# Performance work log

Measured on AMD Instinct MI355X. Metric: run time of the kernel, lower is better.

Reference implementation:

```python
import jax, jax.numpy as jnp
import numpy as np

K = 128
T_X = 4
DATA_LENGTH = 512
B_GROUPS = 64
B = B_GROUPS * DATA_LENGTH
INV_SQRT2 = 0.7071067811865476  # 1/sqrt(2), haar reconstruction filter coeff


def setup_inputs() -> dict:
    key = jax.random.key(0)
    ks = jax.random.split(key, 9)
    x = jax.random.normal(ks[0], (B, T_X, K), jnp.float32)
    y = jax.random.normal(ks[1], (B, 1, K), jnp.float32)
    s = 1.0 / np.sqrt(K).astype(np.float32)
    Wq = jax.random.normal(ks[2], (K, K), jnp.float32) * s
    Wk = jax.random.normal(ks[3], (K, K), jnp.float32) * s
    Wv = jax.random.normal(ks[4], (K, K), jnp.float32) * s
    conv_w = jax.random.normal(ks[5], (K, 2 * K), jnp.float32) * (1.0 / np.sqrt(2 * K).astype(np.float32))
    conv_b = jax.random.normal(ks[6], (K,), jnp.float32) * 0.01
    bn_gamma = jnp.ones((K,), jnp.float32)
    bn_beta = jnp.zeros((K,), jnp.float32)
    bn_mean = jax.random.normal(ks[7], (K,), jnp.float32) * 0.1
    bn_var = jax.random.uniform(ks[8], (K,), jnp.float32, 0.5, 1.5)
    return dict(x=x, y=y, Wq=Wq, Wk=Wk, Wv=Wv, conv_w=conv_w, conv_b=conv_b,
                bn_gamma=bn_gamma, bn_beta=bn_beta, bn_mean=bn_mean, bn_var=bn_var,
                data_length=DATA_LENGTH)


def _idwt_haar(L, H):
    # inverse 1D haar transform along last dim: (Bg, C, 1, T) -> (Bg, C, 1, 2T)
    even = (L + H) * INV_SQRT2
    odd = (L - H) * INV_SQRT2
    out = jnp.stack([even, odd], axis=-1)  # (..., T, 2)
    return out.reshape(L.shape[:-1] + (L.shape[-1] * 2,))


def reference(x, y, Wq, Wk, Wv, conv_w, conv_b, bn_gamma, bn_beta, bn_mean, bn_var, data_length):
    b, t_x, k = x.shape  # t_x = 4 bands, heads = 1, t_y = 1
    q = jnp.einsum('btk,ok->bto', y, Wq)                      # (b, 1, k)
    keys = jnp.einsum('bsk,ok->bso', x, Wk) * (1.0 / (k ** 0.5))  # (b, 4, k)
    v = jnp.einsum('bsk,ok->bso', x, Wv)                      # (b, 4, k)
    dot = jnp.einsum('bto,bso->bs', q, keys)                  # (b, 4)
    w = jax.nn.softmax(dot, axis=1)                           # softmax over the 4 bands
    outs = w[:, :, None] * v                                  # (b, 4, k) band-weighted values
    Bg = b // data_length
    # per band: (b, k) -> (Bg, dl, 1, k) -> permute -> (Bg, k, 1, dl)
    o = outs.reshape(Bg, data_length, t_x, k).transpose(2, 0, 3, 1)  # (4, Bg, k, dl)
    o = o[:, :, :, None, :]                                   # (4, Bg, k, 1, dl)
    out_L = _idwt_haar(o[0], o[1])                            # (Bg, k, 1, 2*dl)
    out_H = _idwt_haar(o[2], o[3])
    out = jnp.concatenate([out_L, out_H], axis=1)             # (Bg, 2k, 1, 2*dl)
    # transition: 1x1 conv + BN (eval mode) + LeakyReLU(0.01)
    z = jnp.einsum('bcij,oc->boij', out, conv_w) + conv_b[None, :, None, None]
    scale = (bn_gamma * jax.lax.rsqrt(bn_var + 1e-5))[None, :, None, None]
    z = (z - bn_mean[None, :, None, None]) * scale + bn_beta[None, :, None, None]
    return jnp.where(z > 0, z, 0.01 * z)
```

## Files before the change

kernel.cpp:

```cpp
#include <hip/hip_runtime.h>
#include <stdint.h>

typedef __attribute__((ext_vector_type(8))) short bf16x8;
typedef __attribute__((ext_vector_type(4))) float f32x4;

__device__ __forceinline__ unsigned short f2bf(float x) {
    union { float f; uint32_t u; } v; v.f = x;
    uint32_t r = v.u + 0x7FFFu + ((v.u >> 16) & 1u);
    return (unsigned short)(r >> 16);
}
__device__ __forceinline__ uint32_t pack2bf(float a, float b) {
    return (uint32_t)f2bf(a) | ((uint32_t)f2bf(b) << 16);
}
__device__ __forceinline__ uint32_t cvtpk(float a, float b) {
    uint32_t r;
    asm("v_cvt_pk_bf16_f32 %0, %1, %2" : "=v"(r) : "v"(a), "v"(b));
    return r;
}
__device__ __forceinline__ float bf2f(uint32_t lo) {
    union { uint32_t u; float f; } v; v.u = lo << 16; return v.f;
}
__device__ __forceinline__ float lrelu(float v) { return v > 0.f ? v : 0.01f * v; }

__global__ __launch_bounds__(256) void precompute_kernel(
    const float* __restrict__ Wq, const float* __restrict__ Wk,
    const float* __restrict__ Wv, const float* __restrict__ conv_w,
    const float* __restrict__ conv_b, const float* __restrict__ bn_gamma,
    const float* __restrict__ bn_beta, const float* __restrict__ bn_mean,
    const float* __restrict__ bn_var,
    unsigned short* __restrict__ Gh, unsigned short* __restrict__ Gl,
    unsigned short* __restrict__ Mh,
    float* __restrict__ scale2, float* __restrict__ bias2)
{
    __shared__ float lds0[2176];
    __shared__ float lds1[2176];
    const int tid = threadIdx.x;
    const int bid = blockIdx.x;

    if (bid == 192) {
        if (tid < 128) {
            float sc = bn_gamma[tid] * rsqrtf(bn_var[tid] + 1e-5f);
            scale2[tid] = sc;
            bias2[tid]  = (conv_b[tid] - bn_mean[tid]) * sc + bn_beta[tid];
        }
        return;
    }

    if (bid < 64) {
        int i0 = (bid >> 3) << 4, j0 = (bid & 7) << 4;
        #pragma unroll
        for (int t = 0; t < 8; ++t) {
            int e = tid + t * 256;
            int o = e >> 4, c = e & 15;
            lds0[o * 17 + c] = Wk[o * 128 + i0 + c];
            lds1[o * 17 + c] = Wq[o * 128 + j0 + c];
        }
        __syncthreads();
        int ti = tid >> 4, tj = tid & 15;
        float sum = 0.f;
        #pragma unroll 8
        for (int o = 0; o < 128; ++o) sum += lds0[o * 17 + ti] * lds1[o * 17 + tj];
        float val = sum * 0.08838834764831845f;
        unsigned short h = f2bf(val);
        int idx = (i0 + ti) * 128 + j0 + tj;
        Gh[idx] = h;
        Gl[idx] = f2bf(val - bf2f(h));
    } else {
        int rel = bid - 64;
        int o0 = (rel >> 4) << 4, c0 = (rel & 15) << 4;
        int cw0 = (c0 >> 7) << 7, cc0 = c0 & 127;
        #pragma unroll
        for (int t = 0; t < 8; ++t) {
            int e = tid + t * 256;
            int to = e >> 7, k = e & 127;
            lds0[to * 132 + k] = conv_w[(o0 + to) * 256 + cw0 + k];
            int kk = e >> 4, c = e & 15;
            lds1[kk * 17 + c] = Wv[kk * 128 + cc0 + c];
        }
        __syncthreads();
        int to = tid >> 4, tc = tid & 15;
        float sum = 0.f;
        #pragma unroll 8
        for (int k = 0; k < 128; ++k) sum += lds0[to * 132 + k] * lds1[k * 17 + tc];
        Mh[(o0 + to) * 256 + c0 + tc] = f2bf(sum * 0.7071067811865476f);
    }
}

#define AADDR(row, gi)   (((row) << 8) + ((((gi) ^ ((row) & 7))) << 4))

__global__ __launch_bounds__(256)
__attribute__((amdgpu_waves_per_eu(3)))
void fused_kernel(
    const float* __restrict__ x, const float* __restrict__ y,
    const unsigned short* __restrict__ Gh, const unsigned short* __restrict__ Gl,
    const unsigned short* __restrict__ Mh,
    const float* __restrict__ scale2, const float* __restrict__ bias2,
    float* __restrict__ out)
{
    __shared__ __align__(16) unsigned char smem[32768];
    float* gbufF = (float*)(smem + 16384);

    const int tid = threadIdx.x;
    const int w = tid >> 6;
    const int l = tid & 63;
    const int quad = l >> 4;
    const int i16 = l & 15;
    const int bid = blockIdx.x;
    const int b0 = bid * 32;

    float4 yv0[2], yv1[2];
    int rowA[2], gkA[2];
    #pragma unroll
    for (int it = 0; it < 2; ++it) {
        int j = tid + it * 256;
        rowA[it] = j >> 4; gkA[it] = j & 15;
        const float* yb = y + (size_t)(b0 + rowA[it]) * 128 + gkA[it] * 8;
        yv0[it] = *(const float4*)(yb);
        yv1[it] = *(const float4*)(yb + 4);
    }
    bf16x8 pgh[4][2], pgl[4][2];
    #pragma unroll
    for (int ks = 0; ks < 4; ++ks) {
        int ksr = (ks + bid) & 3;
        #pragma unroll
        for (int n = 0; n < 2; ++n) {
            int off = ((2 * w + n) * 16 + i16) * 128 + ksr * 32 + quad * 8;
            pgh[ks][n] = *(const bf16x8*)(Gh + off);
            pgl[ks][n] = *(const bf16x8*)(Gl + off);
        }
    }
    union F8 { float4 v[2]; float f[8]; };
    F8 X[2][4];
    #pragma unroll
    for (int pass = 0; pass < 2; ++pass) {
        int b_loc = 8 * w + pass * 4 + quad;
        const float* xb = x + (size_t)(b0 + b_loc) * 512 + i16 * 8;
        #pragma unroll
        for (int t = 0; t < 4; ++t) {
            X[pass][t].v[0] = *(const float4*)(xb + t * 128);
            X[pass][t].v[1] = *(const float4*)(xb + t * 128 + 4);
        }
    }

    #pragma unroll
    for (int it = 0; it < 2; ++it) {
        float f[8] = {yv0[it].x, yv0[it].y, yv0[it].z, yv0[it].w,
                      yv1[it].x, yv1[it].y, yv1[it].z, yv1[it].w};
        uint32_t hi[4], lo[4];
        #pragma unroll
        for (int e = 0; e < 4; ++e) {
            unsigned short h0 = f2bf(f[2 * e]), h1 = f2bf(f[2 * e + 1]);
            hi[e] = (uint32_t)h0 | ((uint32_t)h1 << 16);
            lo[e] = (uint32_t)f2bf(f[2 * e] - bf2f(h0)) |
                    ((uint32_t)f2bf(f[2 * e + 1] - bf2f(h1)) << 16);
        }
        int addr = AADDR(rowA[it], gkA[it]);
        *(uint4*)(smem + addr)        = make_uint4(hi[0], hi[1], hi[2], hi[3]);
        *(uint4*)(smem + 8192 + addr) = make_uint4(lo[0], lo[1], lo[2], lo[3]);
    }
    __syncthreads();

    {
        f32x4 accg[2][2];
        #pragma unroll
        for (int rt = 0; rt < 2; ++rt)
            #pragma unroll
            for (int n = 0; n < 2; ++n) accg[rt][n] = (f32x4){0.f, 0.f, 0.f, 0.f};
        #pragma unroll
        for (int ks = 0; ks < 4; ++ks) {
            int ksr = (ks + bid) & 3;
            bf16x8 ah[2], al[2];
            #pragma unroll
            for (int rt = 0; rt < 2; ++rt) {
                int row = 16 * rt + i16;
                int addr = AADDR(row, ksr * 4 + quad);
                ah[rt] = *(const bf16x8*)(smem + addr);
                al[rt] = *(const bf16x8*)(smem + 8192 + addr);
            }
            #pragma unroll
            for (int n = 0; n < 2; ++n) {
                #pragma unroll
                for (int rt = 0; rt < 2; ++rt) {
                    accg[rt][n] = __builtin_amdgcn_mfma_f32_16x16x32_bf16(ah[rt], pgh[ks][n], accg[rt][n], 0, 0, 0);
                    accg[rt][n] = __builtin_amdgcn_mfma_f32_16x16x32_bf16(al[rt], pgh[ks][n], accg[rt][n], 0, 0, 0);
                    accg[rt][n] = __builtin_amdgcn_mfma_f32_16x16x32_bf16(ah[rt], pgl[ks][n], accg[rt][n], 0, 0, 0);
                }
            }
        }
        #pragma unroll
        for (int n = 0; n < 2; ++n) {
            int i = (2 * w + n) * 16 + i16;
            #pragma unroll
            for (int rt = 0; rt < 2; ++rt)
                #pragma unroll
                for (int r = 0; r < 4; ++r)
                    gbufF[(16 * rt + quad * 4 + r) * 128 + i] = accg[rt][n][r];
        }
    }
    __syncthreads();

    #pragma unroll
    for (int pass = 0; pass < 2; ++pass) {
        int b_loc = 8 * w + pass * 4 + quad;
        float4 ga = *(const float4*)(gbufF + b_loc * 128 + i16 * 8);
        float4 gb = *(const float4*)(gbufF + b_loc * 128 + i16 * 8 + 4);
        float p[4];
        #pragma unroll
        for (int t = 0; t < 4; ++t) {
            float4 a = X[pass][t].v[0], b = X[pass][t].v[1];
            p[t] = a.x * ga.x + a.y * ga.y + a.z * ga.z + a.w * ga.w
                 + b.x * gb.x + b.y * gb.y + b.z * gb.z + b.w * gb.w;
        }
        #pragma unroll
        for (int off = 8; off >= 1; off >>= 1) {
            p[0] += __shfl_xor(p[0], off);
            p[1] += __shfl_xor(p[1], off);
            p[2] += __shfl_xor(p[2], off);
            p[3] += __shfl_xor(p[3], off);
        }
        float mx = fmaxf(fmaxf(p[0], p[1]), fmaxf(p[2], p[3]));
        float e0 = __expf(p[0] - mx), e1 = __expf(p[1] - mx);
        float e2 = __expf(p[2] - mx), e3 = __expf(p[3] - mx);
        float inv = 1.f / (e0 + e1 + e2 + e3);
        float w0 = e0 * inv, w1 = e1 * inv, w2 = e2 * inv, w3 = e3 * inv;
        int r0 = 2 * b_loc, r1 = r0 + 1;
        int a0 = AADDR(r0, i16), a1 = AADDR(r1, i16);
        uint32_t eL[4], oL[4], eH[4], oH[4];
        #pragma unroll
        for (int e = 0; e < 4; ++e) {
            int c0 = 2 * e, c1 = 2 * e + 1;
            eL[e] = cvtpk(w0 * X[pass][0].f[c0] + w1 * X[pass][1].f[c0], w0 * X[pass][0].f[c1] + w1 * X[pass][1].f[c1]);
            oL[e] = cvtpk(w0 * X[pass][0].f[c0] - w1 * X[pass][1].f[c0], w0 * X[pass][0].f[c1] - w1 * X[pass][1].f[c1]);
            eH[e] = cvtpk(w2 * X[pass][2].f[c0] + w3 * X[pass][3].f[c0], w2 * X[pass][2].f[c1] + w3 * X[pass][3].f[c1]);
            oH[e] = cvtpk(w2 * X[pass][2].f[c0] - w3 * X[pass][3].f[c0], w2 * X[pass][2].f[c1] - w3 * X[pass][3].f[c1]);
        }
        *(uint4*)(smem + a0)         = make_uint4(eL[0], eL[1], eL[2], eL[3]);
        *(uint4*)(smem + a1)         = make_uint4(oL[0], oL[1], oL[2], oL[3]);
        *(uint4*)(smem + 16384 + a0) = make_uint4(eH[0], eH[1], eH[2], eH[3]);
        *(uint4*)(smem + 16384 + a1) = make_uint4(oH[0], oH[1], oH[2], oH[3]);
    }

    const int ks0b = bid & 7;
    bf16x8 pmh[2];
    {
        int half = ks0b >> 2, kk = ks0b & 3;
        #pragma unroll
        for (int n = 0; n < 2; ++n)
            pmh[n] = *(const bf16x8*)(Mh + ((2 * w + n) * 16 + i16) * 256 + half * 128 + kk * 32 + quad * 8);
    }
    __syncthreads();

    f32x4 acc[4][2];
    #pragma unroll
    for (int rb = 0; rb < 4; ++rb)
        #pragma unroll
        for (int n = 0; n < 2; ++n) acc[rb][n] = (f32x4){0.f, 0.f, 0.f, 0.f};

    #pragma unroll
    for (int ks = 0; ks < 8; ++ks) {
        int ksr = (ks + bid) & 7;
        int half = ksr >> 2, kk = ksr & 3;
        int base = half << 14;
        int gi = kk * 4 + quad;
        bf16x8 a[4];
        #pragma unroll
        for (int rb = 0; rb < 4; ++rb)
            a[rb] = *(const bf16x8*)(smem + base + AADDR(16 * rb + i16, gi));
        #pragma unroll
        for (int n = 0; n < 2; ++n) {
            bf16x8 bh;
            if (ks == 0) bh = pmh[n];
            else bh = *(const bf16x8*)(Mh + ((2 * w + n) * 16 + i16) * 256 + half * 128 + kk * 32 + quad * 8);
            #pragma unroll
            for (int rb = 0; rb < 4; ++rb)
                acc[rb][n] = __builtin_amdgcn_mfma_f32_16x16x32_bf16(a[rb], bh, acc[rb][n], 0, 0, 0);
        }
    }

    {
        float* outp = out + (size_t)(bid >> 4) * 131072 + (bid & 15) * 64;
        #pragma unroll
        for (int n = 0; n < 2; ++n) {
            int o = (2 * w + n) * 16 + i16;
            float sc = scale2[o], bi = bias2[o];
            #pragma unroll
            for (int rb = 0; rb < 4; ++rb) {
                int jb = 16 * rb + quad * 4;
                f32x4 a = acc[rb][n];
                float4 r;
                r.x = lrelu(a[0] * sc + bi);
                r.y = lrelu(a[1] * sc + bi);
                r.z = lrelu(a[2] * sc + bi);
                r.w = lrelu(a[3] * sc + bi);
                *(float4*)(outp + (size_t)o * 1024 + jb) = r;
            }
        }
    }
}

extern "C" void kernel_launch(void* const* d_in, const int* in_sizes, int n_in,
                              void* d_out, int out_size, void* d_ws, size_t ws_size,
                              hipStream_t stream)
{
    (void)in_sizes; (void)n_in; (void)out_size; (void)ws_size;
    const float* x        = (const float*)d_in[0];
    const float* y        = (const float*)d_in[1];
    const float* Wq       = (const float*)d_in[2];
    const float* Wk       = (const float*)d_in[3];
    const float* Wv       = (const float*)d_in[4];
    const float* conv_w   = (const float*)d_in[5];
    const float* conv_b   = (const float*)d_in[6];
    const float* bn_gamma = (const float*)d_in[7];
    const float* bn_beta  = (const float*)d_in[8];
    const float* bn_mean  = (const float*)d_in[9];
    const float* bn_var   = (const float*)d_in[10];

    unsigned char* ws = (unsigned char*)d_ws;
    unsigned short* Gh = (unsigned short*)(ws);
    unsigned short* Gl = (unsigned short*)(ws + 32768);
    unsigned short* Mh = (unsigned short*)(ws + 65536);
    float* scale2      = (float*)(ws + 131072);
    float* bias2       = (float*)(ws + 131584);

    hipLaunchKernelGGL(precompute_kernel, dim3(193), dim3(256), 0, stream,
                       Wq, Wk, Wv, conv_w, conv_b, bn_gamma, bn_beta, bn_mean,
                       bn_var, Gh, Gl, Mh, scale2, bias2);
    hipLaunchKernelGGL(fused_kernel, dim3(1024), dim3(256), 0, stream,
                       x, y, Gh, Gl, Mh, scale2, bias2, (float*)d_out);
}
```

Measured before the change: 149.5 us.

## Split fused kernel into softmax-weight kernel and IDWT/conv kernel

Result: slower. 156.7 us (+4.8%).

```diff
diff --git a/kernel.cpp b/kernel.cpp
--- a/kernel.cpp
+++ b/kernel.cpp
@@ -8,9 +8,6 @@
     union { float f; uint32_t u; } v; v.f = x;
     uint32_t r = v.u + 0x7FFFu + ((v.u >> 16) & 1u);
     return (unsigned short)(r >> 16);
-}
-__device__ __forceinline__ uint32_t pack2bf(float a, float b) {
-    return (uint32_t)f2bf(a) | ((uint32_t)f2bf(b) << 16);
 }
 __device__ __forceinline__ uint32_t cvtpk(float a, float b) {
     uint32_t r;
@@ -89,13 +86,11 @@
 #define AADDR(row, gi)   (((row) << 8) + ((((gi) ^ ((row) & 7))) << 4))
 
 __global__ __launch_bounds__(256)
-__attribute__((amdgpu_waves_per_eu(3)))
-void fused_kernel(
+__attribute__((amdgpu_waves_per_eu(4)))
+void dot_kernel(
     const float* __restrict__ x, const float* __restrict__ y,
     const unsigned short* __restrict__ Gh, const unsigned short* __restrict__ Gl,
-    const unsigned short* __restrict__ Mh,
-    const float* __restrict__ scale2, const float* __restrict__ bias2,
-    float* __restrict__ out)
+    float* __restrict__ wbuf)
 {
     __shared__ __align__(16) unsigned char smem[32768];
     float* gbufF = (float*)(smem + 16384);
@@ -127,18 +122,6 @@
             int off = ((2 * w + n) * 16 + i16) * 128 + ksr * 32 + quad * 8;
             pgh[ks][n] = *(const bf16x8*)(Gh + off);
             pgl[ks][n] = *(const bf16x8*)(Gl + off);
-        }
-    }
-    union F8 { float4 v[2]; float f[8]; };
-    F8 X[2][4];
-    #pragma unroll
-    for (int pass = 0; pass < 2; ++pass) {
-        int b_loc = 8 * w + pass * 4 + quad;
-        const float* xb = x + (size_t)(b0 + b_loc) * 512 + i16 * 8;
-        #pragma unroll
-        for (int t = 0; t < 4; ++t) {
-            X[pass][t].v[0] = *(const float4*)(xb + t * 128);
-            X[pass][t].v[1] = *(const float4*)(xb + t * 128 + 4);
         }
     }
 
@@ -204,10 +187,12 @@
         int b_loc = 8 * w + pass * 4 + quad;
         float4 ga = *(const float4*)(gbufF + b_loc * 128 + i16 * 8);
         float4 gb = *(const float4*)(gbufF + b_loc * 128 + i16 * 8 + 4);
+        const float* xb = x + (size_t)(b0 + b_loc) * 512 + i16 * 8;
         float p[4];
         #pragma unroll
         for (int t = 0; t < 4; ++t) {
-            float4 a = X[pass][t].v[0], b = X[pass][t].v[1];
+            float4 a = *(const float4*)(xb + t * 128);
+            float4 b = *(const float4*)(xb + t * 128 + 4);
             p[t] = a.x * ga.x + a.y * ga.y + a.z * ga.z + a.w * ga.w
                  + b.x * gb.x + b.y * gb.y + b.z * gb.z + b.w * gb.w;
         }
@@ -222,17 +207,52 @@
         float e0 = __expf(p[0] - mx), e1 = __expf(p[1] - mx);
         float e2 = __expf(p[2] - mx), e3 = __expf(p[3] - mx);
         float inv = 1.f / (e0 + e1 + e2 + e3);
-        float w0 = e0 * inv, w1 = e1 * inv, w2 = e2 * inv, w3 = e3 * inv;
+        if (i16 == 0) {
+            float4 wv = make_float4(e0 * inv, e1 * inv, e2 * inv, e3 * inv);
+            *(float4*)(wbuf + (size_t)(b0 + b_loc) * 4) = wv;
+        }
+    }
+}
+
+__global__ __launch_bounds__(256) void u_kernel(
+    const float* __restrict__ x, const float* __restrict__ wbuf,
+    const unsigned short* __restrict__ Mh,
+    const float* __restrict__ scale2, const float* __restrict__ bias2,
+    float* __restrict__ out)
+{
+    __shared__ __align__(16) unsigned char smem[32768];
+    const int tid = threadIdx.x;
+    const int w = tid >> 6;
+    const int l = tid & 63;
+    const int quad = l >> 4;
+    const int i16 = l & 15;
+    const int bid = blockIdx.x;
+    const int b0 = bid * 32;
+
+    union F8 { float4 v[2]; float f[8]; };
+
+    #pragma unroll
+    for (int pass = 0; pass < 2; ++pass) {
+        int b_loc = 8 * w + pass * 4 + quad;
+        float4 wv = *(const float4*)(wbuf + (size_t)(b0 + b_loc) * 4);
+        const float* xb = x + (size_t)(b0 + b_loc) * 512 + i16 * 8;
+        F8 X[4];
+        #pragma unroll
+        for (int t = 0; t < 4; ++t) {
+            X[t].v[0] = *(const float4*)(xb + t * 128);
+            X[t].v[1] = *(const float4*)(xb + t * 128 + 4);
+        }
+        float w0 = wv.x, w1 = wv.y, w2 = wv.z, w3 = wv.w;
         int r0 = 2 * b_loc, r1 = r0 + 1;
         int a0 = AADDR(r0, i16), a1 = AADDR(r1, i16);
         uint32_t eL[4], oL[4], eH[4], oH[4];
         #pragma unroll
         for (int e = 0; e < 4; ++e) {
             int c0 = 2 * e, c1 = 2 * e + 1;
-            eL[e] = cvtpk(w0 * X[pass][0].f[c0] + w1 * X[pass][1].f[c0], w0 * X[pass][0].f[c1] + w1 * X[pass][1].f[c1]);
-            oL[e] = cvtpk(w0 * X[pass][0].f[c0] - w1 * X[pass][1].f[c0], w0 * X[pass][0].f[c1] - w1 * X[pass][1].f[c1]);
-            eH[e] = cvtpk(w2 * X[pass][2].f[c0] + w3 * X[pass][3].f[c0], w2 * X[pass][2].f[c1] + w3 * X[pass][3].f[c1]);
-            oH[e] = cvtpk(w2 * X[pass][2].f[c0] - w3 * X[pass][3].f[c0], w2 * X[pass][2].f[c1] - w3 * X[pass][3].f[c1]);
+            eL[e] = cvtpk(w0 * X[0].f[c0] + w1 * X[1].f[c0], w0 * X[0].f[c1] + w1 * X[1].f[c1]);
+            oL[e] = cvtpk(w0 * X[0].f[c0] - w1 * X[1].f[c0], w0 * X[0].f[c1] - w1 * X[1].f[c1]);
+            eH[e] = cvtpk(w2 * X[2].f[c0] + w3 * X[3].f[c0], w2 * X[2].f[c1] + w3 * X[3].f[c1]);
+            oH[e] = cvtpk(w2 * X[2].f[c0] - w3 * X[3].f[c0], w2 * X[2].f[c1] - w3 * X[3].f[c1]);
         }
         *(uint4*)(smem + a0)         = make_uint4(eL[0], eL[1], eL[2], eL[3]);
         *(uint4*)(smem + a1)         = make_uint4(oL[0], oL[1], oL[2], oL[3]);
@@ -321,10 +341,13 @@
     unsigned short* Mh = (unsigned short*)(ws + 65536);
     float* scale2      = (float*)(ws + 131072);
     float* bias2       = (float*)(ws + 131584);
+    float* wbuf        = (float*)(ws + 132096);
 
     hipLaunchKernelGGL(precompute_kernel, dim3(193), dim3(256), 0, stream,
                        Wq, Wk, Wv, conv_w, conv_b, bn_gamma, bn_beta, bn_mean,
                        bn_var, Gh, Gl, Mh, scale2, bias2);
-    hipLaunchKernelGGL(fused_kernel, dim3(1024), dim3(256), 0, stream,
-                       x, y, Gh, Gl, Mh, scale2, bias2, (float*)d_out);
-}
+    hipLaunchKernelGGL(dot_kernel, dim3(1024), dim3(256), 0, stream,
+                       x, y, Gh, Gl, wbuf);
+    hipLaunchKernelGGL(u_kernel, dim3(1024), dim3(256), 0, stream,
+                       x, wbuf, Mh, scale2, bias2, (float*)d_out);
+}
```

## Issue global loads via inline asm with explicit vmcnt waits to overlap phases

Applied to the files above, without the earlier changes.

Result: slower. 153.3 us (+2.6%).

```diff
diff --git a/kernel.cpp b/kernel.cpp
--- a/kernel.cpp
+++ b/kernel.cpp
@@ -9,9 +9,6 @@
     uint32_t r = v.u + 0x7FFFu + ((v.u >> 16) & 1u);
     return (unsigned short)(r >> 16);
 }
-__device__ __forceinline__ uint32_t pack2bf(float a, float b) {
-    return (uint32_t)f2bf(a) | ((uint32_t)f2bf(b) << 16);
-}
 __device__ __forceinline__ uint32_t cvtpk(float a, float b) {
     uint32_t r;
     asm("v_cvt_pk_bf16_f32 %0, %1, %2" : "=v"(r) : "v"(a), "v"(b));
@@ -21,6 +18,21 @@
     union { uint32_t u; float f; } v; v.u = lo << 16; return v.f;
 }
 __device__ __forceinline__ float lrelu(float v) { return v > 0.f ? v : 0.01f * v; }
+
+__device__ __forceinline__ f32x4 ald4(const float* p) {
+    f32x4 d;
+    asm volatile("global_load_dwordx4 %0, %1, off" : "=&v"(d) : "v"(p) : "memory");
+    return d;
+}
+__device__ __forceinline__ bf16x8 bld8(const unsigned short* p) {
+    bf16x8 d;
+    asm volatile("global_load_dwordx4 %0, %1, off" : "=&v"(d) : "v"(p) : "memory");
+    return d;
+}
+#define WAITV(N) do { asm volatile("s_waitcnt vmcnt(" #N ")" ::: "memory"); \
+                      __builtin_amdgcn_sched_barrier(0); } while (0)
+#define BARRIER() do { asm volatile("s_waitcnt lgkmcnt(0)\n\ts_barrier" ::: "memory"); \
+                       __builtin_amdgcn_sched_barrier(0); } while (0)
 
 __global__ __launch_bounds__(256) void precompute_kernel(
     const float* __restrict__ Wq, const float* __restrict__ Wk,
@@ -89,7 +101,7 @@
 #define AADDR(row, gi)   (((row) << 8) + ((((gi) ^ ((row) & 7))) << 4))
 
 __global__ __launch_bounds__(256)
-__attribute__((amdgpu_waves_per_eu(3)))
+__attribute__((amdgpu_waves_per_eu(2)))
 void fused_kernel(
     const float* __restrict__ x, const float* __restrict__ y,
     const unsigned short* __restrict__ Gh, const unsigned short* __restrict__ Gl,
@@ -108,15 +120,15 @@
     const int bid = blockIdx.x;
     const int b0 = bid * 32;
 
-    float4 yv0[2], yv1[2];
     int rowA[2], gkA[2];
+    f32x4 yv0[2], yv1[2];
     #pragma unroll
     for (int it = 0; it < 2; ++it) {
         int j = tid + it * 256;
         rowA[it] = j >> 4; gkA[it] = j & 15;
         const float* yb = y + (size_t)(b0 + rowA[it]) * 128 + gkA[it] * 8;
-        yv0[it] = *(const float4*)(yb);
-        yv1[it] = *(const float4*)(yb + 4);
+        yv0[it] = ald4(yb);
+        yv1[it] = ald4(yb + 4);
     }
     bf16x8 pgh[4][2], pgl[4][2];
     #pragma unroll
@@ -125,27 +137,27 @@
         #pragma unroll
         for (int n = 0; n < 2; ++n) {
             int off = ((2 * w + n) * 16 + i16) * 128 + ksr * 32 + quad * 8;
-            pgh[ks][n] = *(const bf16x8*)(Gh + off);
-            pgl[ks][n] = *(const bf16x8*)(Gl + off);
-        }
-    }
-    union F8 { float4 v[2]; float f[8]; };
-    F8 X[2][4];
+            pgh[ks][n] = bld8(Gh + off);
+            pgl[ks][n] = bld8(Gl + off);
+        }
+    }
+    f32x4 X0[2][4], X1[2][4];
     #pragma unroll
     for (int pass = 0; pass < 2; ++pass) {
         int b_loc = 8 * w + pass * 4 + quad;
         const float* xb = x + (size_t)(b0 + b_loc) * 512 + i16 * 8;
         #pragma unroll
         for (int t = 0; t < 4; ++t) {
-            X[pass][t].v[0] = *(const float4*)(xb + t * 128);
-            X[pass][t].v[1] = *(const float4*)(xb + t * 128 + 4);
-        }
-    }
-
+            X0[pass][t] = ald4(xb + t * 128);
+            X1[pass][t] = ald4(xb + t * 128 + 4);
+        }
+    }
+
+    WAITV(32);
     #pragma unroll
     for (int it = 0; it < 2; ++it) {
-        float f[8] = {yv0[it].x, yv0[it].y, yv0[it].z, yv0[it].w,
-                      yv1[it].x, yv1[it].y, yv1[it].z, yv1[it].w};
+        float f[8] = {yv0[it][0], yv0[it][1], yv0[it][2], yv0[it][3],
+                      yv1[it][0], yv1[it][1], yv1[it][2], yv1[it][3]};
         uint32_t hi[4], lo[4];
         #pragma unroll
         for (int e = 0; e < 4; ++e) {
@@ -158,8 +170,9 @@
         *(uint4*)(smem + addr)        = make_uint4(hi[0], hi[1], hi[2], hi[3]);
         *(uint4*)(smem + 8192 + addr) = make_uint4(lo[0], lo[1], lo[2], lo[3]);
     }
-    __syncthreads();
-
+    BARRIER();
+
+    WAITV(16);
     {
         f32x4 accg[2][2];
         #pragma unroll
@@ -197,19 +210,25 @@
                     gbufF[(16 * rt + quad * 4 + r) * 128 + i] = accg[rt][n][r];
         }
     }
-    __syncthreads();
-
+    BARRIER();
+
+    WAITV(0);
     #pragma unroll
     for (int pass = 0; pass < 2; ++pass) {
         int b_loc = 8 * w + pass * 4 + quad;
         float4 ga = *(const float4*)(gbufF + b_loc * 128 + i16 * 8);
         float4 gb = *(const float4*)(gbufF + b_loc * 128 + i16 * 8 + 4);
+        float xf[4][8];
         float p[4];
         #pragma unroll
         for (int t = 0; t < 4; ++t) {
-            float4 a = X[pass][t].v[0], b = X[pass][t].v[1];
-            p[t] = a.x * ga.x + a.y * ga.y + a.z * ga.z + a.w * ga.w
-                 + b.x * gb.x + b.y * gb.y + b.z * gb.z + b.w * gb.w;
+            #pragma unroll
+            for (int e = 0; e < 4; ++e) {
+                xf[t][e]     = X0[pass][t][e];
+                xf[t][4 + e] = X1[pass][t][e];
+            }
+            p[t] = xf[t][0] * ga.x + xf[t][1] * ga.y + xf[t][2] * ga.z + xf[t][3] * ga.w
+                 + xf[t][4] * gb.x + xf[t][5] * gb.y + xf[t][6] * gb.z + xf[t][7] * gb.w;
         }
         #pragma unroll
         for (int off = 8; off >= 1; off >>= 1) {
@@ -229,10 +248,10 @@
         #pragma unroll
         for (int e = 0; e < 4; ++e) {
             int c0 = 2 * e, c1 = 2 * e + 1;
-            eL[e] = cvtpk(w0 * X[pass][0].f[c0] + w1 * X[pass][1].f[c0], w0 * X[pass][0].f[c1] + w1 * X[pass][1].f[c1]);
-            oL[e] = cvtpk(w0 * X[pass][0].f[c0] - w1 * X[pass][1].f[c0], w0 * X[pass][0].f[c1] - w1 * X[pass][1].f[c1]);
-            eH[e] = cvtpk(w2 * X[pass][2].f[c0] + w3 * X[pass][3].f[c0], w2 * X[pass][2].f[c1] + w3 * X[pass][3].f[c1]);
-            oH[e] = cvtpk(w2 * X[pass][2].f[c0] - w3 * X[pass][3].f[c0], w2 * X[pass][2].f[c1] - w3 * X[pass][3].f[c1]);
+            eL[e] = cvtpk(w0 * xf[0][c0] + w1 * xf[1][c0], w0 * xf[0][c1] + w1 * xf[1][c1]);
+            oL[e] = cvtpk(w0 * xf[0][c0] - w1 * xf[1][c0], w0 * xf[0][c1] - w1 * xf[1][c1]);
+            eH[e] = cvtpk(w2 * xf[2][c0] + w3 * xf[3][c0], w2 * xf[2][c1] + w3 * xf[3][c1]);
+            oH[e] = cvtpk(w2 * xf[2][c0] - w3 * xf[3][c0], w2 * xf[2][c1] - w3 * xf[3][c1]);
         }
         *(uint4*)(smem + a0)         = make_uint4(eL[0], eL[1], eL[2], eL[3]);
         *(uint4*)(smem + a1)         = make_uint4(oL[0], oL[1], oL[2], oL[3]);
@@ -248,7 +267,7 @@
         for (int n = 0; n < 2; ++n)
             pmh[n] = *(const bf16x8*)(Mh + ((2 * w + n) * 16 + i16) * 256 + half * 128 + kk * 32 + quad * 8);
     }
-    __syncthreads();
+    BARRIER();
 
     f32x4 acc[4][2];
     #pragma unroll
```
